# Kernel tuning notes

Measured on AMD Instinct MI355X. Metric: run time of the kernel, lower is better.

The kernel has to match this reference:

```python
import jax, jax.numpy as jnp
import numpy as np

C1, C2, C3, C4, C5 = 20, 100, 500, 2000, 10000
FEAT, B = 512, 8192
# parent maps (stand-ins for l1_to_l2..l4_to_l5 group lists): child c -> parent c // fanout
P5 = jnp.arange(C5) // 5   # l5 class -> l4 group
P4 = jnp.arange(C4) // 4   # l4 class -> l3 group
P3 = jnp.arange(C3) // 5   # l3 class -> l2 group
P2 = jnp.arange(C2) // 5   # l2 class -> l1 group


def _l2norm(w):
    # F.normalize(w, p=2, dim=1)
    return w / jnp.maximum(jnp.linalg.norm(w, axis=1, keepdims=True), 1e-12)


def _jsd(p, q, eps=1e-8):
    # Jensen-Shannon divergence between row-wise distributions, mean over batch
    m = 0.5 * (p + q)
    log_m = jnp.log(m + eps)
    kl_pm = jnp.sum(p * (jnp.log(p + eps) - log_m), axis=1)
    kl_qm = jnp.sum(q * (jnp.log(q + eps) - log_m), axis=1)
    return jnp.mean(0.5 * (kl_pm + kl_qm))


def setup_inputs() -> dict:
    key = jax.random.key(0)
    k = jax.random.split(key, 8)
    s = 0.02
    return {
        "x": jax.random.normal(k[0], (B, FEAT), jnp.float32),
        "targets": jax.random.randint(k[1], (B,), 0, C5, jnp.int32),
        "W1": jax.random.normal(k[2], (C1, FEAT), jnp.float32) * s,
        "b1": jnp.zeros((C1,), jnp.float32),
        "W2": jax.random.normal(k[3], (C2, FEAT), jnp.float32) * s,
        "b2": jnp.zeros((C2,), jnp.float32),
        "W3": jax.random.normal(k[4], (C3, FEAT), jnp.float32) * s,
        "b3": jnp.zeros((C3,), jnp.float32),
        "W4": jax.random.normal(k[5], (C4, FEAT), jnp.float32) * s,
        "b4": jnp.zeros((C4,), jnp.float32),
        "W5": jax.random.normal(k[6], (C5, FEAT), jnp.float32) * s,
        "b5": jnp.zeros((C5,), jnp.float32),
    }


def reference(x, targets, W1, b1, W2, b2, W3, b3, W4, b4, W5, b5):
    # row-normalized classifier weights (second F.normalize in the original is idempotent)
    w1, w2, w3, w4, w5 = (_l2norm(W1), _l2norm(W2), _l2norm(W3), _l2norm(W4), _l2norm(W5))
    l1 = x @ w1.T + b1
    l2 = x @ w2.T + b2
    l3 = x @ w3.T + b3
    l4 = x @ w4.T + b4
    l5 = x @ w5.T + b5  # [B, C5]

    # cross-entropy on finest level logits
    logp5 = jax.nn.log_softmax(l5, axis=1)
    ce_loss = -jnp.mean(jnp.take_along_axis(logp5, targets[:, None].astype(jnp.int32), axis=1)[:, 0])

    p1 = jax.nn.softmax(l1, axis=1)
    p2 = jax.nn.softmax(l2, axis=1)
    p3 = jax.nn.softmax(l3, axis=1)
    p4 = jax.nn.softmax(l4, axis=1)
    p5 = jax.nn.softmax(l5, axis=1)

    # hierarchy-aggregated weights: segment-sum child rows, renormalize, cosine vs parent
    def agg_cos(parent_w, child_w, seg, num_seg):
        hat = _l2norm(jax.ops.segment_sum(child_w, seg, num_segments=num_seg))
        return jnp.mean(jnp.sum(parent_w * hat, axis=1))  # rows are unit norm -> cosine

    l2_w_45 = agg_cos(w4, w5, P5, C4)
    l2_w_34 = agg_cos(w3, w4, P4, C3)
    l2_w_23 = agg_cos(w2, w3, P3, C2)
    l2_w_12 = agg_cos(w1, w2, P2, C1)

    # hierarchy-aggregated probabilities: column segment-sums, then JSD vs parent
    def agg_prob(child_p, seg, num_seg):
        return jax.ops.segment_sum(child_p.T, seg, num_segments=num_seg).T

    jsd_45 = _jsd(agg_prob(p5, P5, C4), p4)
    jsd_34 = _jsd(agg_prob(p4, P4, C3), p3)
    jsd_23 = _jsd(agg_prob(p3, P3, C2), p2)
    jsd_12 = _jsd(agg_prob(p2, P2, C1), p1)

    loss = ce_loss + (jsd_45 + jsd_34 + jsd_23 + jsd_12) - (l2_w_45 + l2_w_34 + l2_w_23 + l2_w_12)
    return p5, loss
```

## Files before the change

kernel.cpp:

```cpp
#include <hip/hip_runtime.h>
#include <hip/hip_bf16.h>
#include <stdint.h>

typedef unsigned short u16;
typedef unsigned char u8;
typedef __bf16 bf16x8 __attribute__((ext_vector_type(8)));
typedef float f32x2 __attribute__((ext_vector_type(2)));
typedef float f32x4 __attribute__((ext_vector_type(4)));
typedef unsigned int u32x4 __attribute__((ext_vector_type(4)));

#define FEAT 512
#define BATCH 8192
#define NC1 20
#define NC2 100
#define NC3 500
#define NC4 2000
#define NC5 10000
#define NCAT 2620
#define LDP 2624
#define NTOT 12620
#define NCT 40
#define WN_BLOCKS 3155
#define CAST_BLOCKS 2048
#define NGRP 2620
#define WCOS_BLOCKS 655

__device__ inline u16 f2bf(float f) {
    unsigned int u = __builtin_bit_cast(unsigned int, f);
    unsigned int r = (u + 0x7FFFu + ((u >> 16) & 1u)) >> 16;
    return (u16)r;
}
__device__ inline float bfu(u16 u) {
    return __builtin_bit_cast(float, (unsigned int)u << 16);
}
__device__ inline unsigned int pack4_fp8(float a0, float a1, float a2, float a3) {
    int v = 0;
    v = __builtin_amdgcn_cvt_pk_fp8_f32(a0, a1, v, false);
    v = __builtin_amdgcn_cvt_pk_fp8_f32(a2, a3, v, true);
    return (unsigned int)v;
}
__device__ inline f32x4 unpack4_fp8(unsigned int v) {
    f32x2 lo = __builtin_amdgcn_cvt_pk_f32_fp8((int)v, false);
    f32x2 hi = __builtin_amdgcn_cvt_pk_f32_fp8((int)v, true);
    f32x4 o; o[0] = lo[0]; o[1] = lo[1]; o[2] = hi[0]; o[3] = hi[1];
    return o;
}
__device__ inline float fp8_1(u8 u) {
    return __builtin_amdgcn_cvt_f32_fp8((int)u, 0);
}

__device__ inline float waveReduceSum(float v) {
    #pragma unroll
    for (int off = 32; off > 0; off >>= 1) v += __shfl_xor(v, off);
    return v;
}
__device__ inline float waveReduceMax(float v) {
    #pragma unroll
    for (int off = 32; off > 0; off >>= 1) v = fmaxf(v, __shfl_xor(v, off));
    return v;
}
__device__ inline float blockReduceSum(float v, float* sh) {
    int t = threadIdx.x;
    v = waveReduceSum(v);
    __syncthreads();
    if ((t & 63) == 0) sh[t >> 6] = v;
    __syncthreads();
    return sh[0] + sh[1] + sh[2] + sh[3];
}
__device__ inline float blockReduceMax(float v, float* sh) {
    int t = threadIdx.x;
    v = waveReduceMax(v);
    __syncthreads();
    if ((t & 63) == 0) sh[t >> 6] = v;
    __syncthreads();
    return fmaxf(fmaxf(sh[0], sh[1]), fmaxf(sh[2], sh[3]));
}

__device__ inline void gload16(const void* g, void* l) {
    __builtin_amdgcn_global_load_lds((const __attribute__((address_space(1))) void*)g,
                                     (__attribute__((address_space(3))) void*)l, 16, 0, 0);
}


__global__ __launch_bounds__(256) void prep(const float* __restrict__ x, u16* __restrict__ xb,
                                            const float* __restrict__ W1, const float* __restrict__ b1,
                                            const float* __restrict__ W2, const float* __restrict__ b2,
                                            const float* __restrict__ W3, const float* __restrict__ b3,
                                            const float* __restrict__ W4, const float* __restrict__ b4,
                                            const float* __restrict__ W5, const float* __restrict__ b5,
                                            u16* __restrict__ wb, float* __restrict__ biascat,
                                            float* __restrict__ c45, float* __restrict__ c34,
                                            float* __restrict__ c23, float* __restrict__ c12) {
    int bid = blockIdx.x;
    if (bid < WN_BLOCKS) {
        int r = bid * 4 + (threadIdx.x >> 6);
        if (r >= NTOT) return;
        int t = threadIdx.x & 63;
        const float* W; const float* b; int lr;
        if      (r < 20)   { W = W1; b = b1; lr = r; }
        else if (r < 120)  { W = W2; b = b2; lr = r - 20; }
        else if (r < 620)  { W = W3; b = b3; lr = r - 120; }
        else if (r < 2620) { W = W4; b = b4; lr = r - 620; }
        else               { W = W5; b = b5; lr = r - 2620; }
        const float* p = W + (size_t)lr * FEAT + t * 8;
        float v[8]; float ss = 0.f;
        #pragma unroll
        for (int j = 0; j < 8; ++j) { v[j] = p[j]; ss += v[j] * v[j]; }
        ss = waveReduceSum(ss);
        float inv = 1.0f / fmaxf(sqrtf(ss), 1e-12f);
        union { u16 u[8]; uint4 q; } o;
        #pragma unroll
        for (int j = 0; j < 8; ++j) o.u[j] = f2bf(v[j] * inv);
        ((uint4*)(wb + (size_t)r * FEAT))[t] = o.q;
        if (t == 0) biascat[r] = b[lr];
    } else if (bid < WN_BLOCKS + CAST_BLOCKS) {
        int i = (bid - WN_BLOCKS) * 256 + threadIdx.x;
        const float* p = x + (size_t)i * 8;
        union { u16 u[8]; uint4 v; } o;
        #pragma unroll
        for (int j = 0; j < 8; ++j) o.u[j] = f2bf(p[j]);
        ((uint4*)xb)[i] = o.v;
    } else {
        int g = (bid - WN_BLOCKS - CAST_BLOCKS) * 4 + (threadIdx.x >> 6);
        if (g >= NGRP) return;
        int t = threadIdx.x & 63;
        const float* Wp; const float* Wc; int fan, j; float* dst;
        if      (g < 2000) { Wp = W4; Wc = W5; fan = 5; dst = c45; j = g; }
        else if (g < 2500) { Wp = W3; Wc = W4; fan = 4; dst = c34; j = g - 2000; }
        else if (g < 2600) { Wp = W2; Wc = W3; fan = 5; dst = c23; j = g - 2500; }
        else               { Wp = W1; Wc = W2; fan = 5; dst = c12; j = g - 2600; }

        float hat[8] = {0, 0, 0, 0, 0, 0, 0, 0};
        for (int c = 0; c < fan; ++c) {
            const float* cr = Wc + ((size_t)(j * fan + c)) * FEAT + t * 8;
            float v[8]; float ss = 0.f;
            #pragma unroll
            for (int i = 0; i < 8; ++i) { v[i] = cr[i]; ss += v[i] * v[i]; }
            ss = waveReduceSum(ss);
            float inv = 1.0f / fmaxf(sqrtf(ss), 1e-12f);
            #pragma unroll
            for (int i = 0; i < 8; ++i) hat[i] += v[i] * inv;
        }
        float hs = 0.f;
        #pragma unroll
        for (int i = 0; i < 8; ++i) hs += hat[i] * hat[i];
        hs = waveReduceSum(hs);
        float hinv = 1.0f / fmaxf(sqrtf(hs), 1e-12f);
        const float* pr = Wp + (size_t)j * FEAT + t * 8;
        float ps = 0.f, dot = 0.f;
        #pragma unroll
        for (int i = 0; i < 8; ++i) { float pv = pr[i]; ps += pv * pv; dot += pv * hat[i]; }
        ps = waveReduceSum(ps);
        dot = waveReduceSum(dot);
        if (t == 0) dst[j] = dot * hinv / fmaxf(sqrtf(ps), 1e-12f);
    }
}


#define BM 256
#define BN 256
#define BK 64
#define KITERS (FEAT / BK)

__global__ __launch_bounds__(512, 2) void gemm_all(const u16* __restrict__ A, const u16* __restrict__ Bw,
                                                   const float* __restrict__ bias,
                                                   u16* __restrict__ pcat, u8* __restrict__ l5f8,
                                                   float* __restrict__ pmax, float* __restrict__ psum) {
    __shared__ u16 sAB[2][2 * BM * BK];
    const int t = threadIdx.x;
    const int lane = t & 63, wid = t >> 6;
    const int lane15 = lane & 15, q = lane >> 4;
    const int wr = wid >> 2, wcol = wid & 3;

    int nwg = gridDim.x * gridDim.y;
    int lid = blockIdx.y * gridDim.x + blockIdx.x;
    int cpx = nwg >> 3;
    int swz = (lid & 7) * cpx + (lid >> 3);
    int bx = swz % gridDim.x, by = swz / gridDim.x;
    const int r0 = bx * BM, c0 = by * BN;

    f32x4 acc[8][4];
    #pragma unroll
    for (int m = 0; m < 8; ++m)
        #pragma unroll
        for (int n = 0; n < 4; ++n) acc[m][n] = f32x4{0.f, 0.f, 0.f, 0.f};

    auto stageHalf = [&](char* nb, int region, int kh, int ktB) {
        #pragma unroll
        for (int p = 0; p < 2; ++p) {
            int c = p * 512 + t;
            int row = c >> 2;
            int srck = ktB + kh * 32 + 8 * ((c & 3) ^ ((c >> 3) & 3));
            const u16* g;
            if (region == 0) {
                g = A + (size_t)(r0 + row) * FEAT + srck;
            } else {
                int br = c0 + row; if (br >= NTOT) br = NTOT - 1;
                g = Bw + (size_t)br * FEAT + srck;
            }
            gload16(g, nb + region * 32768 + kh * 16384 + (size_t)c * 16);
        }
    };

    auto readA = [&](char* sb, int ks, int mh, bf16x8* af) {
        #pragma unroll
        for (int i = 0; i < 4; ++i) {
            int row = wr * 128 + (mh * 4 + i) * 16 + lane15;
            af[i] = *reinterpret_cast<const bf16x8*>(sb + ks * 16384 + row * 64 +
                                                     16 * ((q ^ (row >> 1)) & 3));
        }
    };
    auto readB = [&](char* sb, int ks, bf16x8* bv) {
        #pragma unroll
        for (int n = 0; n < 4; ++n) {
            int row = wcol * 64 + n * 16 + lane15;
            bv[n] = *reinterpret_cast<const bf16x8*>(sb + 32768 + ks * 16384 + row * 64 +
                                                     16 * ((q ^ (row >> 1)) & 3));
        }
    };

    {
        char* nb = (char*)sAB[0];
        stageHalf(nb, 0, 0, 0);
        stageHalf(nb, 1, 0, 0);
        stageHalf(nb, 0, 1, 0);
        stageHalf(nb, 1, 1, 0);
    }

    for (int T = 0; T < KITERS; ++T) {
        char* sb = (char*)sAB[T & 1];
        char* nb = (char*)sAB[(T + 1) & 1];
        const bool more = (T + 1 < KITERS);
        const int ktB = (T + 1) * BK;

        asm volatile("s_waitcnt vmcnt(4)" ::: "memory");
        __builtin_amdgcn_sched_barrier(0);
        __builtin_amdgcn_s_barrier();
        __builtin_amdgcn_sched_barrier(0);
        {
            bf16x8 bv[4], af[4];
            readB(sb, 0, bv);
            readA(sb, 0, 0, af);
            if (more) stageHalf(nb, 0, 0, ktB);
            __builtin_amdgcn_sched_barrier(0);
            __builtin_amdgcn_s_setprio(1);
            #pragma unroll
            for (int i = 0; i < 4; ++i)
                #pragma unroll
                for (int n = 0; n < 4; ++n)
                    acc[i][n] = __builtin_amdgcn_mfma_f32_16x16x32_bf16(bv[n], af[i], acc[i][n], 0, 0, 0);
            __builtin_amdgcn_s_setprio(0);
            __builtin_amdgcn_sched_barrier(0);
            readA(sb, 0, 1, af);
            if (more) stageHalf(nb, 1, 0, ktB);
            __builtin_amdgcn_sched_barrier(0);
            __builtin_amdgcn_s_setprio(1);
            #pragma unroll
            for (int i = 0; i < 4; ++i)
                #pragma unroll
                for (int n = 0; n < 4; ++n)
                    acc[4 + i][n] = __builtin_amdgcn_mfma_f32_16x16x32_bf16(bv[n], af[i], acc[4 + i][n], 0, 0, 0);
            __builtin_amdgcn_s_setprio(0);
            __builtin_amdgcn_sched_barrier(0);
        }

        if (more) { asm volatile("s_waitcnt vmcnt(4)" ::: "memory"); }
        else      { asm volatile("s_waitcnt vmcnt(0)" ::: "memory"); }
        __builtin_amdgcn_sched_barrier(0);
        __builtin_amdgcn_s_barrier();
        __builtin_amdgcn_sched_barrier(0);
        {
            bf16x8 bv[4], af[4];
            readB(sb, 1, bv);
            readA(sb, 1, 0, af);
            if (more) stageHalf(nb, 0, 1, ktB);
            __builtin_amdgcn_sched_barrier(0);
            __builtin_amdgcn_s_setprio(1);
            #pragma unroll
            for (int i = 0; i < 4; ++i)
                #pragma unroll
                for (int n = 0; n < 4; ++n)
                    acc[i][n] = __builtin_amdgcn_mfma_f32_16x16x32_bf16(bv[n], af[i], acc[i][n], 0, 0, 0);
            __builtin_amdgcn_s_setprio(0);
            __builtin_amdgcn_sched_barrier(0);
            readA(sb, 1, 1, af);
            if (more) stageHalf(nb, 1, 1, ktB);
            __builtin_amdgcn_sched_barrier(0);
            __builtin_amdgcn_s_setprio(1);
            #pragma unroll
            for (int i = 0; i < 4; ++i)
                #pragma unroll
                for (int n = 0; n < 4; ++n)
                    acc[4 + i][n] = __builtin_amdgcn_mfma_f32_16x16x32_bf16(bv[n], af[i], acc[4 + i][n], 0, 0, 0);
            __builtin_amdgcn_s_setprio(0);
            __builtin_amdgcn_sched_barrier(0);
        }
    }

    bool vld[4], svld[4]; int cb[4];
    #pragma unroll
    for (int n = 0; n < 4; ++n) {
        cb[n] = c0 + wcol * 64 + n * 16 + q * 4;
        vld[n] = (cb[n] < NTOT);
        svld[n] = vld[n] && (cb[n] >= NCAT);
        if (vld[n]) {
            float b0 = bias[cb[n]], b1 = bias[cb[n] + 1], b2 = bias[cb[n] + 2], b3 = bias[cb[n] + 3];
            #pragma unroll
            for (int m = 0; m < 8; ++m) {
                acc[m][n][0] += b0; acc[m][n][1] += b1;
                acc[m][n][2] += b2; acc[m][n][3] += b3;
            }
        }
    }

    if (by >= 10) {
        float* fmx = (float*)sAB;
        float* fsm = fmx + 1024;
        float bm[8];
        #pragma unroll
        for (int m = 0; m < 8; ++m) {
            float v = -1e30f;
            #pragma unroll
            for (int n = 0; n < 4; ++n)
                if (svld[n]) {
                    #pragma unroll
                    for (int j = 0; j < 4; ++j) v = fmaxf(v, acc[m][n][j]);
                }
            v = fmaxf(v, __shfl_xor(v, 16));
            v = fmaxf(v, __shfl_xor(v, 32));
            bm[m] = v;
        }
        __syncthreads();
        if (lane < 16) {
            #pragma unroll
            for (int m = 0; m < 8; ++m)
                fmx[(wr * 128 + m * 16 + lane15) * 4 + wcol] = bm[m];
        }
        __syncthreads();
        #pragma unroll
        for (int m = 0; m < 8; ++m) {
            int row = wr * 128 + m * 16 + lane15;
            bm[m] = fmaxf(fmaxf(fmx[row * 4], fmx[row * 4 + 1]),
                          fmaxf(fmx[row * 4 + 2], fmx[row * 4 + 3]));
        }
        float sm[8];
        #pragma unroll
        for (int m = 0; m < 8; ++m) {
            float s = 0.f;
            #pragma unroll
            for (int n = 0; n < 4; ++n)
                if (svld[n]) {
                    #pragma unroll
                    for (int j = 0; j < 4; ++j) s += __expf(acc[m][n][j] - bm[m]);
                }
            s += __shfl_xor(s, 16);
            s += __shfl_xor(s, 32);
            sm[m] = s;
        }
        if (lane < 16) {
            #pragma unroll
            for (int m = 0; m < 8; ++m)
                fsm[(wr * 128 + m * 16 + lane15) * 4 + wcol] = sm[m];
        }
        __syncthreads();
        if (t < 256) {
            float m4 = fmaxf(fmaxf(fmx[t * 4], fmx[t * 4 + 1]), fmaxf(fmx[t * 4 + 2], fmx[t * 4 + 3]));
            float s4 = fsm[t * 4] + fsm[t * 4 + 1] + fsm[t * 4 + 2] + fsm[t * 4 + 3];
            size_t idx = (size_t)(r0 + t) * NCT + (by - 10);
            pmax[idx] = m4;
            psum[idx] = s4;
        }
    }

    #pragma unroll
    for (int m = 0; m < 8; ++m) {
        int row = r0 + wr * 128 + m * 16 + lane15;
        #pragma unroll
        for (int n = 0; n < 4; ++n) {
            if (vld[n]) {
                if (cb[n] < NCAT) {
                    union { u16 u[4]; uint2 v; } pk;
                    #pragma unroll
                    for (int j = 0; j < 4; ++j) pk.u[j] = f2bf(acc[m][n][j]);
                    *reinterpret_cast<uint2*>(&pcat[(size_t)row * LDP + cb[n]]) = pk.v;
                } else {
                    unsigned int v = pack4_fp8(acc[m][n][0], acc[m][n][1], acc[m][n][2], acc[m][n][3]);
                    *reinterpret_cast<unsigned int*>(&l5f8[(size_t)row * NC5 + (cb[n] - NCAT)]) = v;
                }
            }
        }
    }
}


__global__ __launch_bounds__(256) void probs_all(const u8* __restrict__ l5f8, float* __restrict__ out,
                                                 const u16* __restrict__ pcat,
                                                 const float* __restrict__ pmax, const float* __restrict__ psum,
                                                 const int* __restrict__ tgt,
                                                 float* __restrict__ cerow,
                                                 float* __restrict__ j12, float* __restrict__ j23,
                                                 float* __restrict__ j34, float* __restrict__ j45) {
    __shared__ u16 P5[NC5];
    __shared__ float PC[LDP];
    __shared__ float sh[4];
    __shared__ float shls;
    int b = blockIdx.x, t = threadIdx.x;
    float* orow = out + (size_t)b * NC5;
    const u8* lrow = l5f8 + (size_t)b * NC5;
    const u16* prow = pcat + (size_t)b * LDP;

    if (t < 64) {
        float pm = (t < NCT) ? pmax[(size_t)b * NCT + t] : -1e30f;
        float ps = (t < NCT) ? psum[(size_t)b * NCT + t] : 0.f;
        float gm = waveReduceMax(pm);
        float s = waveReduceSum(ps * __expf(pm - gm));
        if (t == 0) {
            float ls = gm + __logf(s);
            shls = ls;
            int tg = tgt[b];
            cerow[b] = -(fp8_1(lrow[tg]) - ls);
        }
    }
    for (int c = t; c < LDP / 8; c += 256) {
        u32x4 raw = __builtin_nontemporal_load(&((const u32x4*)prow)[c]);
        const u16* rp = (const u16*)&raw;
        #pragma unroll
        for (int k = 0; k < 8; ++k) PC[c * 8 + k] = bfu(rp[k]);
    }
    __syncthreads();
    float ls = shls;

    for (int c = t; c < NC5 / 8; c += 256) {
        uint2 raw = ((const uint2*)lrow)[c];
        f32x4 l0 = unpack4_fp8(raw.x);
        f32x4 l1 = unpack4_fp8(raw.y);
        f32x4 o0, o1;
        #pragma unroll
        for (int k = 0; k < 4; ++k) o0[k] = __expf(l0[k] - ls);
        #pragma unroll
        for (int k = 0; k < 4; ++k) o1[k] = __expf(l1[k] - ls);
        __builtin_nontemporal_store(o0, &((f32x4*)orow)[c * 2]);
        __builtin_nontemporal_store(o1, &((f32x4*)orow)[c * 2 + 1]);
        union { u16 u[8]; uint4 v; } pk;
        #pragma unroll
        for (int k = 0; k < 4; ++k) pk.u[k] = f2bf(o0[k]);
        #pragma unroll
        for (int k = 0; k < 4; ++k) pk.u[4 + k] = f2bf(o1[k]);
        ((uint4*)P5)[c] = pk.v;
    }
    __syncthreads();

    auto softmax_seg = [&](int off, int C) {
        float m = -1e30f;
        for (int c = t; c < C; c += 256) m = fmaxf(m, PC[off + c]);
        m = blockReduceMax(m, sh);
        float s = 0.f;
        for (int c = t; c < C; c += 256) { float e = __expf(PC[off + c] - m); PC[off + c] = e; s += e; }
        s = blockReduceSum(s, sh);
        float inv = 1.0f / s;
        for (int c = t; c < C; c += 256) PC[off + c] *= inv;
    };
    softmax_seg(0, NC1);
    softmax_seg(20, NC2);
    softmax_seg(120, NC3);
    softmax_seg(620, NC4);
    __syncthreads();

    {
        float klpm = 0.f, klqm = 0.f;
        for (int g = t; g < NC4; g += 256) {
            float qv = 0.f;
            #pragma unroll
            for (int f = 0; f < 5; ++f) qv += bfu(P5[5 * g + f]);
            float pp = PC[620 + g];
            float mm = 0.5f * (qv + pp);
            float lm = __logf(mm + 1e-8f);
            klpm += qv * (__logf(qv + 1e-8f) - lm);
            klqm += pp * (__logf(pp + 1e-8f) - lm);
        }
        float tot = blockReduceSum(0.5f * (klpm + klqm), sh);
        if (t == 0) j45[b] = tot;
    }
    auto jsd_seg = [&](int childOff, int fan, int parentOff, int nPar, float* dst) {
        float klpm = 0.f, klqm = 0.f;
        for (int g = t; g < nPar; g += 256) {
            float qv = 0.f;
            for (int f = 0; f < fan; ++f) qv += PC[childOff + g * fan + f];
            float pp = PC[parentOff + g];
            float mm = 0.5f * (qv + pp);
            float lm = __logf(mm + 1e-8f);
            klpm += qv * (__logf(qv + 1e-8f) - lm);
            klqm += pp * (__logf(pp + 1e-8f) - lm);
        }
        float tot = blockReduceSum(0.5f * (klpm + klqm), sh);
        if (t == 0) dst[b] = tot;
    };
    jsd_seg(620, 4, 120, NC3, j34);
    jsd_seg(120, 5, 20, NC2, j23);
    jsd_seg(20, 5, 0, NC1, j12);
}

__global__ __launch_bounds__(256) void finalize(const float* __restrict__ ce, const float* __restrict__ j45,
                                                const float* __restrict__ j34, const float* __restrict__ j23,
                                                const float* __restrict__ j12, const float* __restrict__ c45,
                                                const float* __restrict__ c34, const float* __restrict__ c23,
                                                const float* __restrict__ c12, float* __restrict__ lossOut) {
    __shared__ float sh[4];
    auto meanArr = [&](const float* a, int n) {
        float s = 0.f;
        for (int i = threadIdx.x; i < n; i += 256) s += a[i];
        s = blockReduceSum(s, sh);
        return s / n;
    };
    float loss = meanArr(ce, BATCH);
    loss += meanArr(j45, BATCH) + meanArr(j34, BATCH) + meanArr(j23, BATCH) + meanArr(j12, BATCH);
    loss -= meanArr(c45, NC4) + meanArr(c34, NC3) + meanArr(c23, NC2) + meanArr(c12, NC1);
    if (threadIdx.x == 0) *lossOut = loss;
}


extern "C" void kernel_launch(void* const* d_in, const int* in_sizes, int n_in,
                              void* d_out, int out_size, void* d_ws, size_t ws_size,
                              hipStream_t stream) {
    const float* x  = (const float*)d_in[0];
    const int*   tg = (const int*)d_in[1];
    const float* W1 = (const float*)d_in[2];  const float* b1 = (const float*)d_in[3];
    const float* W2 = (const float*)d_in[4];  const float* b2 = (const float*)d_in[5];
    const float* W3 = (const float*)d_in[6];  const float* b3 = (const float*)d_in[7];
    const float* W4 = (const float*)d_in[8];  const float* b4 = (const float*)d_in[9];
    const float* W5 = (const float*)d_in[10]; const float* b5 = (const float*)d_in[11];
    float* out = (float*)d_out;

    char* ws = (char*)d_ws;
    size_t off = 0;
    auto alloc = [&](size_t bytes) { void* p = ws + off; off = (off + bytes + 255) & ~(size_t)255; return p; };
    u16*   xb      = (u16*)alloc((size_t)BATCH * FEAT * 2);
    u16*   wb      = (u16*)alloc((size_t)NTOT * FEAT * 2);
    float* biascat = (float*)alloc((size_t)NTOT * 4);
    u16*   pcat    = (u16*)alloc((size_t)BATCH * LDP * 2);
    u8*    l5f8    = (u8*)alloc((size_t)BATCH * NC5);
    float* pmax    = (float*)alloc((size_t)BATCH * NCT * 4);
    float* psum    = (float*)alloc((size_t)BATCH * NCT * 4);
    float* cerow   = (float*)alloc((size_t)BATCH * 4);
    float* j45     = (float*)alloc((size_t)BATCH * 4);
    float* j34     = (float*)alloc((size_t)BATCH * 4);
    float* j23     = (float*)alloc((size_t)BATCH * 4);
    float* j12     = (float*)alloc((size_t)BATCH * 4);
    float* c45     = (float*)alloc((size_t)NC4 * 4);
    float* c34     = (float*)alloc((size_t)NC3 * 4);
    float* c23     = (float*)alloc((size_t)NC2 * 4);
    float* c12     = (float*)alloc((size_t)NC1 * 4);

    prep<<<WN_BLOCKS + CAST_BLOCKS + WCOS_BLOCKS, 256, 0, stream>>>(
        x, xb, W1, b1, W2, b2, W3, b3, W4, b4, W5, b5, wb, biascat, c45, c34, c23, c12);

    gemm_all<<<dim3(BATCH / BM, (NTOT + BN - 1) / BN), 512, 0, stream>>>(
        xb, wb, biascat, pcat, l5f8, pmax, psum);

    probs_all<<<BATCH, 256, 0, stream>>>(l5f8, out, pcat, pmax, psum, tg, cerow,
                                         j12, j23, j34, j45);

    finalize<<<1, 256, 0, stream>>>(cerow, j45, j34, j23, j12, c45, c34, c23, c12,
                                    out + (size_t)BATCH * NC5);
}
```

Before: 368.8 us.

## Switch main GEMM inputs from bf16 to fp8 with fp8 MFMA

Casts x and the normalized weights to fp8 in prep and runs the fused logits GEMM with the fp8 16x16x32 MFMA. The LDS staging layout, swizzle, load counts and waitcnt values are reworked to match the halved operand width. This halves operand bytes in global memory and LDS and uses the fp8 matrix path, but it lowers logit precision, which feeds softmax, cross-entropy and JSD and may break tolerance. Unscaled x values in fp8 e4m3 lose considerable precision.

```diff
diff --git a/kernel.cpp b/kernel.cpp
--- a/kernel.cpp
+++ b/kernel.cpp
@@ -4,7 +4,7 @@
 
 typedef unsigned short u16;
 typedef unsigned char u8;
-typedef __bf16 bf16x8 __attribute__((ext_vector_type(8)));
+typedef long i64;
 typedef float f32x2 __attribute__((ext_vector_type(2)));
 typedef float f32x4 __attribute__((ext_vector_type(4)));
 typedef unsigned int u32x4 __attribute__((ext_vector_type(4)));
@@ -82,13 +82,13 @@
 }
 
 
-__global__ __launch_bounds__(256) void prep(const float* __restrict__ x, u16* __restrict__ xb,
+__global__ __launch_bounds__(256) void prep(const float* __restrict__ x, u8* __restrict__ xb8,
                                             const float* __restrict__ W1, const float* __restrict__ b1,
                                             const float* __restrict__ W2, const float* __restrict__ b2,
                                             const float* __restrict__ W3, const float* __restrict__ b3,
                                             const float* __restrict__ W4, const float* __restrict__ b4,
                                             const float* __restrict__ W5, const float* __restrict__ b5,
-                                            u16* __restrict__ wb, float* __restrict__ biascat,
+                                            u8* __restrict__ wb8, float* __restrict__ biascat,
                                             float* __restrict__ c45, float* __restrict__ c34,
                                             float* __restrict__ c23, float* __restrict__ c12) {
     int bid = blockIdx.x;
@@ -108,18 +108,18 @@
         for (int j = 0; j < 8; ++j) { v[j] = p[j]; ss += v[j] * v[j]; }
         ss = waveReduceSum(ss);
         float inv = 1.0f / fmaxf(sqrtf(ss), 1e-12f);
-        union { u16 u[8]; uint4 q; } o;
-        #pragma unroll
-        for (int j = 0; j < 8; ++j) o.u[j] = f2bf(v[j] * inv);
-        ((uint4*)(wb + (size_t)r * FEAT))[t] = o.q;
+        uint2 o;
+        o.x = pack4_fp8(v[0] * inv, v[1] * inv, v[2] * inv, v[3] * inv);
+        o.y = pack4_fp8(v[4] * inv, v[5] * inv, v[6] * inv, v[7] * inv);
+        *reinterpret_cast<uint2*>(wb8 + (size_t)r * FEAT + t * 8) = o;
         if (t == 0) biascat[r] = b[lr];
     } else if (bid < WN_BLOCKS + CAST_BLOCKS) {
         int i = (bid - WN_BLOCKS) * 256 + threadIdx.x;
         const float* p = x + (size_t)i * 8;
-        union { u16 u[8]; uint4 v; } o;
-        #pragma unroll
-        for (int j = 0; j < 8; ++j) o.u[j] = f2bf(p[j]);
-        ((uint4*)xb)[i] = o.v;
+        uint2 o;
+        o.x = pack4_fp8(p[0], p[1], p[2], p[3]);
+        o.y = pack4_fp8(p[4], p[5], p[6], p[7]);
+        *reinterpret_cast<uint2*>(xb8 + (size_t)i * 8) = o;
     } else {
         int g = (bid - WN_BLOCKS - CAST_BLOCKS) * 4 + (threadIdx.x >> 6);
         if (g >= NGRP) return;
@@ -162,11 +162,11 @@
 #define BK 64
 #define KITERS (FEAT / BK)
 
-__global__ __launch_bounds__(512, 2) void gemm_all(const u16* __restrict__ A, const u16* __restrict__ Bw,
+__global__ __launch_bounds__(512, 2) void gemm_all(const u8* __restrict__ A, const u8* __restrict__ Bw,
                                                    const float* __restrict__ bias,
                                                    u16* __restrict__ pcat, u8* __restrict__ l5f8,
                                                    float* __restrict__ pmax, float* __restrict__ psum) {
-    __shared__ u16 sAB[2][2 * BM * BK];
+    __shared__ uint4 sABq[2][2048];
     const int t = threadIdx.x;
     const int lane = t & 63, wid = t >> 6;
     const int lane15 = lane & 15, q = lane >> 4;
@@ -185,113 +185,109 @@
         #pragma unroll
         for (int n = 0; n < 4; ++n) acc[m][n] = f32x4{0.f, 0.f, 0.f, 0.f};
 
-    auto stageHalf = [&](char* nb, int region, int kh, int ktB) {
-        #pragma unroll
-        for (int p = 0; p < 2; ++p) {
-            int c = p * 512 + t;
-            int row = c >> 2;
-            int srck = ktB + kh * 32 + 8 * ((c & 3) ^ ((c >> 3) & 3));
-            const u16* g;
-            if (region == 0) {
-                g = A + (size_t)(r0 + row) * FEAT + srck;
-            } else {
-                int br = c0 + row; if (br >= NTOT) br = NTOT - 1;
-                g = Bw + (size_t)br * FEAT + srck;
-            }
-            gload16(g, nb + region * 32768 + kh * 16384 + (size_t)c * 16);
-        }
+    auto stageUnit = [&](char* nb, int region, int kh, int ktB) {
+        int row = t >> 1, p = t & 1;
+        int srck = ktB + kh * 32 + 16 * (p ^ (row & 1));
+        const u8* g;
+        if (region == 0) {
+            g = A + (size_t)(r0 + row) * FEAT + srck;
+        } else {
+            int br = c0 + row; if (br >= NTOT) br = NTOT - 1;
+            g = Bw + (size_t)br * FEAT + srck;
+        }
+        gload16(g, nb + region * 16384 + kh * 8192 + (size_t)t * 16);
     };
 
-    auto readA = [&](char* sb, int ks, int mh, bf16x8* af) {
+    auto readA = [&](char* sb, int ks, int mh, i64* af) {
         #pragma unroll
         for (int i = 0; i < 4; ++i) {
             int row = wr * 128 + (mh * 4 + i) * 16 + lane15;
-            af[i] = *reinterpret_cast<const bf16x8*>(sb + ks * 16384 + row * 64 +
-                                                     16 * ((q ^ (row >> 1)) & 3));
+            af[i] = *reinterpret_cast<const i64*>(sb + ks * 8192 + row * 32 +
+                                                  16 * ((q >> 1) ^ (row & 1)) + 8 * (q & 1));
         }
     };
-    auto readB = [&](char* sb, int ks, bf16x8* bv) {
+    auto readB = [&](char* sb, int ks, i64* bv) {
         #pragma unroll
         for (int n = 0; n < 4; ++n) {
             int row = wcol * 64 + n * 16 + lane15;
-            bv[n] = *reinterpret_cast<const bf16x8*>(sb + 32768 + ks * 16384 + row * 64 +
-                                                     16 * ((q ^ (row >> 1)) & 3));
+            bv[n] = *reinterpret_cast<const i64*>(sb + 16384 + ks * 8192 + row * 32 +
+                                                  16 * ((q >> 1) ^ (row & 1)) + 8 * (q & 1));
         }
     };
 
     {
-        char* nb = (char*)sAB[0];
-        stageHalf(nb, 0, 0, 0);
-        stageHalf(nb, 1, 0, 0);
-        stageHalf(nb, 0, 1, 0);
-        stageHalf(nb, 1, 1, 0);
+        char* nb = (char*)sABq[0];
+        stageUnit(nb, 0, 0, 0);
+        stageUnit(nb, 1, 0, 0);
+        stageUnit(nb, 0, 1, 0);
+        stageUnit(nb, 1, 1, 0);
     }
 
     for (int T = 0; T < KITERS; ++T) {
-        char* sb = (char*)sAB[T & 1];
-        char* nb = (char*)sAB[(T + 1) & 1];
+        char* sb = (char*)sABq[T & 1];
+        char* nb = (char*)sABq[(T + 1) & 1];
         const bool more = (T + 1 < KITERS);
         const int ktB = (T + 1) * BK;
 
-        asm volatile("s_waitcnt vmcnt(4)" ::: "memory");
+        asm volatile("s_waitcnt vmcnt(2)" ::: "memory");
         __builtin_amdgcn_sched_barrier(0);
         __builtin_amdgcn_s_barrier();
         __builtin_amdgcn_sched_barrier(0);
         {
-            bf16x8 bv[4], af[4];
+            i64 bv[4], af[4];
             readB(sb, 0, bv);
             readA(sb, 0, 0, af);
-            if (more) stageHalf(nb, 0, 0, ktB);
+            if (more) stageUnit(nb, 0, 0, ktB);
             __builtin_amdgcn_sched_barrier(0);
             __builtin_amdgcn_s_setprio(1);
             #pragma unroll
             for (int i = 0; i < 4; ++i)
                 #pragma unroll
                 for (int n = 0; n < 4; ++n)
-                    acc[i][n] = __builtin_amdgcn_mfma_f32_16x16x32_bf16(bv[n], af[i], acc[i][n], 0, 0, 0);
+                    acc[i][n] = __builtin_amdgcn_mfma_f32_16x16x32_fp8_fp8(bv[n], af[i], acc[i][n], 0, 0, 0);
             __builtin_amdgcn_s_setprio(0);
             __builtin_amdgcn_sched_barrier(0);
             readA(sb, 0, 1, af);
-            if (more) stageHalf(nb, 1, 0, ktB);
+            if (more) stageUnit(nb, 1, 0, ktB);
             __builtin_amdgcn_sched_barrier(0);
             __builtin_amdgcn_s_setprio(1);
             #pragma unroll
             for (int i = 0; i < 4; ++i)
                 #pragma unroll
                 for (int n = 0; n < 4; ++n)
-                    acc[4 + i][n] = __builtin_amdgcn_mfma_f32_16x16x32_bf16(bv[n], af[i], acc[4 + i][n], 0, 0, 0);
+                    acc[4 + i][n] = __builtin_amdgcn_mfma_f32_16x16x32_fp8_fp8(bv[n], af[i], acc[4 + i][n], 0, 0, 0);
             __builtin_amdgcn_s_setprio(0);
             __builtin_amdgcn_sched_barrier(0);
         }
 
-        if (more) { asm volatile("s_waitcnt vmcnt(4)" ::: "memory"); }
+        if (more) { asm volatile("s_waitcnt vmcnt(2)" ::: "memory"); }
         else      { asm volatile("s_waitcnt vmcnt(0)" ::: "memory"); }
         __builtin_amdgcn_sched_barrier(0);
         __builtin_amdgcn_s_barrier();
         __builtin_amdgcn_sched_barrier(0);
         {
-            bf16x8 bv[4], af[4];
+            i64 bv[4], af[4];
             readB(sb, 1, bv);
             readA(sb, 1, 0, af);
-            if (more) stageHalf(nb, 0, 1, ktB);
+            if (more) stageUnit(nb, 0, 1, ktB);
             __builtin_amdgcn_sched_barrier(0);
             __builtin_amdgcn_s_setprio(1);
             #pragma unroll
             for (int i = 0; i < 4; ++i)
                 #pragma unroll
                 for (int n = 0; n < 4; ++n)
-                    acc[i][n] = __builtin_amdgcn_mfma_f32_16x16x32_bf16(bv[n], af[i], acc[i][n], 0, 0, 0);
+                    acc[i][n] = __builtin_amdgcn_mfma_f32_16x16x32_fp8_fp8(bv[n], af[i], acc[i][n], 0, 0, 0);
             __builtin_amdgcn_s_setprio(0);
             __builtin_amdgcn_sched_barrier(0);
             readA(sb, 1, 1, af);
-            if (more) stageHalf(nb, 1, 1, ktB);
+            if (more) stageUnit(nb, 1, 1, ktB);
             __builtin_amdgcn_sched_barrier(0);
             __builtin_amdgcn_s_setprio(1);
             #pragma unroll
             for (int i = 0; i < 4; ++i)
                 #pragma unroll
                 for (int n = 0; n < 4; ++n)
-                    acc[4 + i][n] = __builtin_amdgcn_mfma_f32_16x16x32_bf16(bv[n], af[i], acc[4 + i][n], 0, 0, 0);
+                    acc[4 + i][n] = __builtin_amdgcn_mfma_f32_16x16x32_fp8_fp8(bv[n], af[i], acc[4 + i][n], 0, 0, 0);
             __builtin_amdgcn_s_setprio(0);
             __builtin_amdgcn_sched_barrier(0);
         }
@@ -314,7 +310,7 @@
     }
 
     if (by >= 10) {
-        float* fmx = (float*)sAB;
+        float* fmx = (float*)sABq;
         float* fsm = fmx + 1024;
         float bm[8];
         #pragma unroll
@@ -534,8 +530,8 @@
     char* ws = (char*)d_ws;
     size_t off = 0;
     auto alloc = [&](size_t bytes) { void* p = ws + off; off = (off + bytes + 255) & ~(size_t)255; return p; };
-    u16*   xb      = (u16*)alloc((size_t)BATCH * FEAT * 2);
-    u16*   wb      = (u16*)alloc((size_t)NTOT * FEAT * 2);
+    u8*    xb8     = (u8*)alloc((size_t)BATCH * FEAT);
+    u8*    wb8     = (u8*)alloc((size_t)NTOT * FEAT);
     float* biascat = (float*)alloc((size_t)NTOT * 4);
     u16*   pcat    = (u16*)alloc((size_t)BATCH * LDP * 2);
     u8*    l5f8    = (u8*)alloc((size_t)BATCH * NC5);
@@ -552,10 +548,10 @@
     float* c12     = (float*)alloc((size_t)NC1 * 4);
 
     prep<<<WN_BLOCKS + CAST_BLOCKS + WCOS_BLOCKS, 256, 0, stream>>>(
-        x, xb, W1, b1, W2, b2, W3, b3, W4, b4, W5, b5, wb, biascat, c45, c34, c23, c12);
+        x, xb8, W1, b1, W2, b2, W3, b3, W4, b4, W5, b5, wb8, biascat, c45, c34, c23, c12);
 
     gemm_all<<<dim3(BATCH / BM, (NTOT + BN - 1) / BN), 512, 0, stream>>>(
-        xb, wb, biascat, pcat, l5f8, pmax, psum);
+        xb8, wb8, biascat, pcat, l5f8, pmax, psum);
 
     probs_all<<<BATCH, 256, 0, stream>>>(l5f8, out, pcat, pmax, psum, tg, cerow,
                                          j12, j23, j34, j45);
```

Result: faster. 356.9 us (-3.2%).
